# Optimization experiments

Hardware: AMD Instinct MI355X
Metric: run time of the kernel (lower is better)

## Reference

```python
import jax, jax.numpy as jnp
import numpy as np

N = 20000
IN_C = 512
HID = 64
H1 = 8
OUT_C = 256
E = 320000
NEG_SLOPE = 0.2


def gat_conv(x, src, dst, W, a_src, a_dst, b, concat):
    # PyG GATConv (shared lin for src/dst), inference mode (no dropout).
    H, C = a_src.shape
    h = (x @ W).reshape(N, H, C)                      # [N,H,C]
    alpha_src = (h * a_src[None]).sum(-1)             # [N,H]
    alpha_dst = (h * a_dst[None]).sum(-1)             # [N,H]
    alpha = jax.nn.leaky_relu(alpha_src[src] + alpha_dst[dst], NEG_SLOPE)  # [E,H]
    # segment softmax over incoming edges of each dst node
    amax = jax.ops.segment_max(alpha, dst, num_segments=N)
    amax = jnp.where(jnp.isfinite(amax), amax, 0.0)
    ex = jnp.exp(alpha - amax[dst])
    denom = jax.ops.segment_sum(ex, dst, num_segments=N)
    coef = ex / (denom[dst] + 1e-16)                  # [E,H]
    msg = h[src] * coef[:, :, None]                   # [E,H,C]
    out = jax.ops.segment_sum(msg, dst, num_segments=N)  # [N,H,C]
    out = out.reshape(N, H * C) if concat else out.mean(axis=1)
    return out + b


def setup_inputs() -> dict:
    key = jax.random.key(0)
    ks = jax.random.split(key, 10)
    x = jax.random.normal(ks[0], (N, IN_C), dtype=jnp.float32)
    edge_index = jax.random.randint(ks[1], (2, E), 0, N, dtype=jnp.int32)
    s1 = 1.0 / np.sqrt(IN_C)
    s2 = 1.0 / np.sqrt(HID * H1)
    W1 = jax.random.uniform(ks[2], (IN_C, H1 * HID), jnp.float32, -s1, s1)
    att_src1 = jax.random.uniform(ks[3], (H1, HID), jnp.float32, -s1, s1)
    att_dst1 = jax.random.uniform(ks[4], (H1, HID), jnp.float32, -s1, s1)
    b1 = jnp.zeros((H1 * HID,), jnp.float32)
    W2 = jax.random.uniform(ks[5], (H1 * HID, OUT_C), jnp.float32, -s2, s2)
    att_src2 = jax.random.uniform(ks[6], (1, OUT_C), jnp.float32, -s2, s2)
    att_dst2 = jax.random.uniform(ks[7], (1, OUT_C), jnp.float32, -s2, s2)
    b2 = jnp.zeros((OUT_C,), jnp.float32)
    return {"x": x, "edge_index": edge_index, "W1": W1, "att_src1": att_src1,
            "att_dst1": att_dst1, "b1": b1, "W2": W2, "att_src2": att_src2,
            "att_dst2": att_dst2, "b2": b2}


def reference(x, edge_index, W1, att_src1, att_dst1, b1, W2, att_src2, att_dst2, b2):
    # add self-loops (PyG GATConv default add_self_loops=True)
    loop = jnp.arange(N, dtype=edge_index.dtype)
    src = jnp.concatenate([edge_index[0], loop])
    dst = jnp.concatenate([edge_index[1], loop])
    h = gat_conv(x, src, dst, W1, att_src1, att_dst1, b1, concat=True)
    h = jax.nn.elu(h)
    out = gat_conv(h, src, dst, W2, att_src2, att_dst2, b2, concat=False)
    return jax.nn.log_softmax(out, axis=1)
```

## Files before the change

kernel.cpp:

```cpp
#include <hip/hip_runtime.h>
#include <math.h>

#define N_NODES 20000
#define NP1     20001
#define IN_CH   512
#define HID_TOT 512
#define OUT_CH  256
#define N_EDGE  320000
#define TOT_EDGE (N_EDGE + N_NODES)
#define EPAD    400000

typedef __attribute__((ext_vector_type(8))) short short8;
typedef __attribute__((ext_vector_type(4))) float f32x4;
typedef __attribute__((ext_vector_type(2))) float f32x2;

__device__ __forceinline__ ushort f2bf(float f) {
    union { float f; unsigned u; } v; v.f = f;
    unsigned u = v.u;
    return (ushort)((u + 0x7fffu + ((u >> 16) & 1u)) >> 16);
}

__device__ __forceinline__ void glds16(const ushort* g, ushort* l) {
    __builtin_amdgcn_global_load_lds(
        (const __attribute__((address_space(1))) void*)g,
        (__attribute__((address_space(3))) void*)l, 16, 0, 0);
}

__device__ __forceinline__ float lrelu(float a) { return fmaxf(a, 0.2f * a); }

#define NA_BLK (N_NODES * IN_CH / 4 / 256)
#define NB_BLK ((IN_CH / 64) * (HID_TOT / 4))
#define NC_BLK ((HID_TOT / 64) * (OUT_CH / 4))
#define NZ_BLK ((N_NODES + 255) / 256)
__global__ __launch_bounds__(256) void prep_kernel(const float* __restrict__ x,
                                                   ushort* __restrict__ xb,
                                                   const float* __restrict__ W1,
                                                   ushort* __restrict__ w1t,
                                                   const float* __restrict__ W2,
                                                   ushort* __restrict__ w2t,
                                                   int* __restrict__ counts,
                                                   float* __restrict__ as1,
                                                   float* __restrict__ as2,
                                                   float* __restrict__ ad2,
                                                   unsigned char* __restrict__ h1f,
                                                   unsigned char* __restrict__ h2f) {
    int b = blockIdx.x;
    int t = threadIdx.x;
    if (b < NA_BLK) {
        int i = b * 256 + t;
        float4 v = *(const float4*)&x[(size_t)i * 4];
        ushort4 o = make_ushort4(f2bf(v.x), f2bf(v.y), f2bf(v.z), f2bf(v.w));
        *(ushort4*)&xb[(size_t)i * 4] = o;
    } else if (b < NA_BLK + NB_BLK) {
        int bb = b - NA_BLK;
        int k = (bb & 7) * 64 + (t & 63);
        int n = (bb >> 3) * 4 + (t >> 6);
        w1t[(size_t)n * IN_CH + k] = f2bf(W1[(size_t)k * HID_TOT + n]);
    } else if (b < NA_BLK + NB_BLK + NC_BLK) {
        int bb = b - NA_BLK - NB_BLK;
        int k = (bb & 7) * 64 + (t & 63);
        int n = (bb >> 3) * 4 + (t >> 6);
        w2t[(size_t)n * HID_TOT + k] = f2bf(W2[(size_t)k * OUT_CH + n]);
    } else {
        int i = (b - NA_BLK - NB_BLK - NC_BLK) * 256 + t;
        if (i < N_NODES) { counts[i] = 0; as2[i] = 0.f; ad2[i] = 0.f; }
        if (i == N_NODES) as2[N_NODES] = -1e30f;
        if (i < 8) as1[(size_t)i * NP1 + N_NODES] = -1e30f;
        if (i < 128) ((unsigned*)(h1f + (size_t)N_NODES * HID_TOT))[i] = 0u;
        if (i < 64)  ((unsigned*)(h2f + (size_t)N_NODES * OUT_CH))[i] = 0u;
    }
}

__global__ void hist_kernel(const int* __restrict__ ei, int* __restrict__ counts) {
    int e = blockIdx.x * blockDim.x + threadIdx.x;
    if (e >= TOT_EDGE) return;
    int d = (e < N_EDGE) ? ei[N_EDGE + e] : (e - N_EDGE);
    atomicAdd(&counts[d], 1);
}

__global__ __launch_bounds__(1024) void scan_kernel(const int* __restrict__ counts,
                                                    int* __restrict__ offsets,
                                                    int* __restrict__ cursors,
                                                    int* __restrict__ srcs,
                                                    int* __restrict__ perm) {
    const int C = (N_NODES + 1023) / 1024;
    int t = threadIdx.x;
    int lane = t & 63, wid = t >> 6;
    int base = t * C;
    int sum = 0;
#pragma unroll
    for (int i = 0; i < C; i++) {
        int idx = base + i;
        if (idx < N_NODES) sum += (counts[idx] + 3) & ~3;
    }
    int val = sum;
#pragma unroll
    for (int off = 1; off < 64; off <<= 1) {
        int y = __shfl_up(val, off);
        if (lane >= off) val += y;
    }
    __shared__ int wsum[16], woff[16], stotal;
    __shared__ int bins[64];
    if (lane == 63) wsum[wid] = val;
    if (t < 64) bins[t] = 0;
    __syncthreads();
    if (t == 0) {
        int r = 0;
        for (int w = 0; w < 16; w++) { woff[w] = r; r += wsum[w]; }
        stotal = r;
    }
    __syncthreads();
    int running = woff[wid] + (val - sum);
#pragma unroll
    for (int i = 0; i < C; i++) {
        int idx = base + i;
        if (idx < N_NODES) {
            offsets[idx] = running;
            cursors[idx] = running;
            int real = counts[idx];
            int padded = (real + 3) & ~3;
            for (int pp = running + real; pp < running + padded; pp++)
                srcs[pp] = N_NODES;
            running += padded;
        }
    }
    if (t == 0) offsets[N_NODES] = stotal;

#pragma unroll
    for (int i = 0; i < C; i++) {
        int idx = base + i;
        if (idx < N_NODES) {
            int d = counts[idx]; if (d > 63) d = 63;
            atomicAdd(&bins[d], 1);
        }
    }
    __syncthreads();
    if (t == 0) {
        int r = 0;
        for (int d = 0; d < 64; d++) { int c = bins[d]; bins[d] = r; r += c; }
    }
    __syncthreads();
#pragma unroll
    for (int i = 0; i < C; i++) {
        int idx = base + i;
        if (idx < N_NODES) {
            int d = counts[idx]; if (d > 63) d = 63;
            int pos = atomicAdd(&bins[d], 1);
            perm[pos] = idx;
        }
    }
}

__global__ void scatter_kernel(const int* __restrict__ ei, int* __restrict__ cursors,
                               int* __restrict__ srcs) {
    int e = blockIdx.x * blockDim.x + threadIdx.x;
    if (e >= TOT_EDGE) return;
    int s, d;
    if (e < N_EDGE) { s = ei[e]; d = ei[N_EDGE + e]; } else { s = e - N_EDGE; d = s; }
    int pos = atomicAdd(&cursors[d], 1);
    srcs[pos] = s;
}

__global__ __launch_bounds__(256, 2) void gemm_mfma_kernel(const ushort* __restrict__ A,
                                                           const ushort* __restrict__ Bt,
                                                           unsigned char* __restrict__ Cf8,
                                                           const float* __restrict__ asrc,
                                                           const float* __restrict__ adst,
                                                           float* __restrict__ as_out,
                                                           float* __restrict__ ad_out,
                                                           int M, int N, int K, int layer1) {
    __shared__ ushort As[128 * 64];
    __shared__ ushort Bs[128 * 64];
    int t = threadIdx.x;
    int lane = t & 63;
    int wave = t >> 6;
    int wr = (wave >> 1) * 64;
    int wc = (wave & 1) * 64;
    int bm = blockIdx.y * 128, bn = blockIdx.x * 128;
    int q = lane >> 4, l15 = lane & 15;

    const ushort* Aptr[4]; ushort* Alds[4];
    const ushort* Bptr[4]; ushort* Blds[4];
#pragma unroll
    for (int k = 0; k < 4; k++) {
        int c = t + 256 * k;
        int r = c >> 3, kqs = c & 7;
        int kqg = kqs ^ (r & 7);
        int ar = bm + r; if (ar >= M) ar = M - 1;
        Aptr[k] = A + (size_t)ar * K + kqg * 8;
        Alds[k] = &As[c * 8];
        Bptr[k] = Bt + (size_t)(bn + r) * K + kqg * 8;
        Blds[k] = &Bs[c * 8];
    }

    f32x4 acc[4][4];
#pragma unroll
    for (int i = 0; i < 4; i++)
#pragma unroll
        for (int j = 0; j < 4; j++) acc[i][j] = f32x4{0.f, 0.f, 0.f, 0.f};

    for (int k0 = 0; k0 < K; k0 += 64) {
        __syncthreads();
        glds16(Aptr[0] + k0, Alds[0]);
        glds16(Aptr[1] + k0, Alds[1]);
        glds16(Aptr[2] + k0, Alds[2]);
        glds16(Aptr[3] + k0, Alds[3]);
        glds16(Bptr[0] + k0, Blds[0]);
        glds16(Bptr[1] + k0, Blds[1]);
        glds16(Bptr[2] + k0, Blds[2]);
        glds16(Bptr[3] + k0, Blds[3]);
        __syncthreads();

#pragma unroll
        for (int s = 0; s < 2; s++) {
            int kq = s * 4 + q;
            short8 af[4], bf[4];
#pragma unroll
            for (int i = 0; i < 4; i++) {
                int row = wr + i * 16 + l15;
                int slot = kq ^ (row & 7);
                af[i] = *(const short8*)&As[row * 64 + slot * 8];
            }
#pragma unroll
            for (int j = 0; j < 4; j++) {
                int row = wc + j * 16 + l15;
                int slot = kq ^ (row & 7);
                bf[j] = *(const short8*)&Bs[row * 64 + slot * 8];
            }
#pragma unroll
            for (int i = 0; i < 4; i++)
#pragma unroll
                for (int j = 0; j < 4; j++)
                    acc[i][j] = __builtin_amdgcn_mfma_f32_16x16x32_bf16(af[i], bf[j], acc[i][j], 0, 0, 0);
        }
    }

    float av[4], dv[4];
#pragma unroll
    for (int j = 0; j < 4; j++) {
        int cg = bn + wc + j * 16 + l15;
        av[j] = asrc[cg];
        dv[j] = adst[cg];
    }
    float ps[4][4], pd[4][4];
#pragma unroll
    for (int i = 0; i < 4; i++)
#pragma unroll
        for (int r = 0; r < 4; r++) {
            float p = 0.f, d = 0.f;
#pragma unroll
            for (int j = 0; j < 4; j++) {
                p = fmaf(acc[i][j][r], av[j], p);
                d = fmaf(acc[i][j][r], dv[j], d);
            }
            ps[i][r] = p; pd[i][r] = d;
        }
#pragma unroll
    for (int off = 1; off < 16; off <<= 1) {
#pragma unroll
        for (int i = 0; i < 4; i++)
#pragma unroll
            for (int r = 0; r < 4; r++) {
                ps[i][r] += __shfl_xor(ps[i][r], off);
                pd[i][r] += __shfl_xor(pd[i][r], off);
            }
    }

    int hidx = blockIdx.x * 2 + (wave & 1);
#pragma unroll
    for (int i = 0; i < 4; i++) {
#pragma unroll
        for (int r = 0; r < 4; r++) {
            int rg = bm + wr + i * 16 + q * 4 + r;
            if (rg < M) {
#pragma unroll
                for (int j = 0; j < 4; j++) {
                    int cg = bn + wc + j * 16 + l15;
                    int w8 = __builtin_amdgcn_cvt_pk_fp8_f32(acc[i][j][r], acc[i][j][r], 0, false);
                    Cf8[(size_t)rg * N + cg] = (unsigned char)(w8 & 0xff);
                }
                if (l15 == 0) {
                    if (layer1) {
                        as_out[(size_t)hidx * NP1 + rg] = ps[i][r];
                        ad_out[(size_t)hidx * NP1 + rg] = pd[i][r];
                    } else {
                        atomicAdd(&as_out[rg], ps[i][r]);
                        atomicAdd(&ad_out[rg], pd[i][r]);
                    }
                }
            }
        }
    }
}

__global__ __launch_bounds__(64) void agg1_kernel(const unsigned char* __restrict__ h1f,
                                                  const float* __restrict__ as1,
                                                  const float* __restrict__ ad1,
                                                  const int* __restrict__ offsets,
                                                  const int* __restrict__ srcs,
                                                  const int* __restrict__ perm,
                                                  const float* __restrict__ b1,
                                                  ushort* __restrict__ h1ab) {
    int b = blockIdx.x;
    int head = b & 7;
    int grp = b >> 3;
    int lane = threadIdx.x;
    int sub = lane >> 3;
    int l8 = lane & 7;
    int v = perm[grp * 8 + sub];
    int cofs = head * 64 + l8 * 8;
    const unsigned char* hb = h1f + cofs;
    const float* as1h = as1 + (size_t)head * NP1;
    float adv = ad1[(size_t)head * NP1 + v];
    int s = offsets[v], e = offsets[v + 1];

    float denom = 0.f;
    float acc[8];
#pragma unroll
    for (int k = 0; k < 8; k++) acc[k] = 0.f;

    int i = s;
    int4 cs0 = {0, 0, 0, 0}, cs1 = {0, 0, 0, 0};
    int csn = N_NODES;
    if (i + 8 <= e) {
        cs0 = *(const int4*)&srcs[i];
        cs1 = *(const int4*)&srcs[i + 4];
        csn = srcs[i + l8];
    }
    while (i + 8 <= e) {
        uint2 r[8];
        r[0] = *(const uint2*)&hb[(size_t)cs0.x * HID_TOT];
        r[1] = *(const uint2*)&hb[(size_t)cs0.y * HID_TOT];
        r[2] = *(const uint2*)&hb[(size_t)cs0.z * HID_TOT];
        r[3] = *(const uint2*)&hb[(size_t)cs0.w * HID_TOT];
        r[4] = *(const uint2*)&hb[(size_t)cs1.x * HID_TOT];
        r[5] = *(const uint2*)&hb[(size_t)cs1.y * HID_TOT];
        r[6] = *(const uint2*)&hb[(size_t)cs1.z * HID_TOT];
        r[7] = *(const uint2*)&hb[(size_t)cs1.w * HID_TOT];
        float aown = as1h[csn];
        int ni = i + 8;
        int4 ns0 = cs0, ns1 = cs1; int nsn = csn;
        if (ni + 8 <= e) {
            ns0 = *(const int4*)&srcs[ni];
            ns1 = *(const int4*)&srcs[ni + 4];
            nsn = srcs[ni + l8];
        }
        float w_own = __expf(lrelu(aown + adv));
        denom += w_own;
        float ww[8];
#pragma unroll
        for (int j = 0; j < 8; j++) ww[j] = __shfl(w_own, (lane & 56) | j);
#pragma unroll
        for (int j = 0; j < 8; j++) {
            f32x2 pa = __builtin_amdgcn_cvt_pk_f32_fp8(r[j].x, false);
            f32x2 pb = __builtin_amdgcn_cvt_pk_f32_fp8(r[j].x, true);
            f32x2 pc = __builtin_amdgcn_cvt_pk_f32_fp8(r[j].y, false);
            f32x2 pdd = __builtin_amdgcn_cvt_pk_f32_fp8(r[j].y, true);
            acc[0] = fmaf(ww[j], pa.x, acc[0]); acc[1] = fmaf(ww[j], pa.y, acc[1]);
            acc[2] = fmaf(ww[j], pb.x, acc[2]); acc[3] = fmaf(ww[j], pb.y, acc[3]);
            acc[4] = fmaf(ww[j], pc.x, acc[4]); acc[5] = fmaf(ww[j], pc.y, acc[5]);
            acc[6] = fmaf(ww[j], pdd.x, acc[6]); acc[7] = fmaf(ww[j], pdd.y, acc[7]);
        }
        cs0 = ns0; cs1 = ns1; csn = nsn; i = ni;
    }
    if (i < e) {
        int4 s0 = *(const int4*)&srcs[i];
        int snt = srcs[i + (l8 & 3)];
        uint2 r[4];
        r[0] = *(const uint2*)&hb[(size_t)s0.x * HID_TOT];
        r[1] = *(const uint2*)&hb[(size_t)s0.y * HID_TOT];
        r[2] = *(const uint2*)&hb[(size_t)s0.z * HID_TOT];
        r[3] = *(const uint2*)&hb[(size_t)s0.w * HID_TOT];
        float w_own = __expf(lrelu(as1h[snt] + adv));
        if (l8 < 4) denom += w_own;
        float ww[4];
#pragma unroll
        for (int j = 0; j < 4; j++) ww[j] = __shfl(w_own, (lane & 56) | j);
#pragma unroll
        for (int j = 0; j < 4; j++) {
            f32x2 pa = __builtin_amdgcn_cvt_pk_f32_fp8(r[j].x, false);
            f32x2 pb = __builtin_amdgcn_cvt_pk_f32_fp8(r[j].x, true);
            f32x2 pc = __builtin_amdgcn_cvt_pk_f32_fp8(r[j].y, false);
            f32x2 pdd = __builtin_amdgcn_cvt_pk_f32_fp8(r[j].y, true);
            acc[0] = fmaf(ww[j], pa.x, acc[0]); acc[1] = fmaf(ww[j], pa.y, acc[1]);
            acc[2] = fmaf(ww[j], pb.x, acc[2]); acc[3] = fmaf(ww[j], pb.y, acc[3]);
            acc[4] = fmaf(ww[j], pc.x, acc[4]); acc[5] = fmaf(ww[j], pc.y, acc[5]);
            acc[6] = fmaf(ww[j], pdd.x, acc[6]); acc[7] = fmaf(ww[j], pdd.y, acc[7]);
        }
    }

    denom += __shfl_xor(denom, 1);
    denom += __shfl_xor(denom, 2);
    denom += __shfl_xor(denom, 4);

    float inv = 1.f / (denom + 1e-16f);
    short8 ov;
#pragma unroll
    for (int k = 0; k < 8; k++) {
        float o = acc[k] * inv + b1[cofs + k];
        o = (o > 0.f) ? o : expm1f(o);
        ov[k] = (short)f2bf(o);
    }
    *(short8*)&h1ab[(size_t)v * HID_TOT + cofs] = ov;
}

__global__ __launch_bounds__(64) void agg2_kernel(const unsigned char* __restrict__ h2f,
                                                  const float* __restrict__ as2,
                                                  const float* __restrict__ ad2,
                                                  const int* __restrict__ offsets,
                                                  const int* __restrict__ srcs,
                                                  const int* __restrict__ perm,
                                                  const float* __restrict__ b2,
                                                  float* __restrict__ out) {
    int lane = threadIdx.x;
    int sub = lane >> 5;
    int l32 = lane & 31;
    int v = perm[blockIdx.x * 2 + sub];
    int c8 = l32 * 8;
    const unsigned char* hb = h2f + c8;
    float adv = ad2[v];
    int s = offsets[v], e = offsets[v + 1];

    float denom = 0.f;
    float acc[8];
#pragma unroll
    for (int k = 0; k < 8; k++) acc[k] = 0.f;

    int i = s;
    int4 cs0 = {0, 0, 0, 0}, cs1 = {0, 0, 0, 0};
    int csn = N_NODES;
    if (i + 8 <= e) {
        cs0 = *(const int4*)&srcs[i];
        cs1 = *(const int4*)&srcs[i + 4];
        csn = srcs[i + (l32 & 7)];
    }
    while (i + 8 <= e) {
        uint2 r[8];
        r[0] = *(const uint2*)&hb[(size_t)cs0.x * OUT_CH];
        r[1] = *(const uint2*)&hb[(size_t)cs0.y * OUT_CH];
        r[2] = *(const uint2*)&hb[(size_t)cs0.z * OUT_CH];
        r[3] = *(const uint2*)&hb[(size_t)cs0.w * OUT_CH];
        r[4] = *(const uint2*)&hb[(size_t)cs1.x * OUT_CH];
        r[5] = *(const uint2*)&hb[(size_t)cs1.y * OUT_CH];
        r[6] = *(const uint2*)&hb[(size_t)cs1.z * OUT_CH];
        r[7] = *(const uint2*)&hb[(size_t)cs1.w * OUT_CH];
        float aown = as2[csn];
        int ni = i + 8;
        int4 ns0 = cs0, ns1 = cs1; int nsn = csn;
        if (ni + 8 <= e) {
            ns0 = *(const int4*)&srcs[ni];
            ns1 = *(const int4*)&srcs[ni + 4];
            nsn = srcs[ni + (l32 & 7)];
        }
        float w_own = __expf(lrelu(aown + adv));
        if (l32 < 8) denom += w_own;
        float ww[8];
#pragma unroll
        for (int j = 0; j < 8; j++) ww[j] = __shfl(w_own, (lane & 32) | j);
#pragma unroll
        for (int j = 0; j < 8; j++) {
            f32x2 pa = __builtin_amdgcn_cvt_pk_f32_fp8(r[j].x, false);
            f32x2 pb = __builtin_amdgcn_cvt_pk_f32_fp8(r[j].x, true);
            f32x2 pc = __builtin_amdgcn_cvt_pk_f32_fp8(r[j].y, false);
            f32x2 pdd = __builtin_amdgcn_cvt_pk_f32_fp8(r[j].y, true);
            acc[0] = fmaf(ww[j], pa.x, acc[0]); acc[1] = fmaf(ww[j], pa.y, acc[1]);
            acc[2] = fmaf(ww[j], pb.x, acc[2]); acc[3] = fmaf(ww[j], pb.y, acc[3]);
            acc[4] = fmaf(ww[j], pc.x, acc[4]); acc[5] = fmaf(ww[j], pc.y, acc[5]);
            acc[6] = fmaf(ww[j], pdd.x, acc[6]); acc[7] = fmaf(ww[j], pdd.y, acc[7]);
        }
        cs0 = ns0; cs1 = ns1; csn = nsn; i = ni;
    }
    if (i < e) {
        int4 s0 = *(const int4*)&srcs[i];
        int snt = srcs[i + (l32 & 3)];
        uint2 r[4];
        r[0] = *(const uint2*)&hb[(size_t)s0.x * OUT_CH];
        r[1] = *(const uint2*)&hb[(size_t)s0.y * OUT_CH];
        r[2] = *(const uint2*)&hb[(size_t)s0.z * OUT_CH];
        r[3] = *(const uint2*)&hb[(size_t)s0.w * OUT_CH];
        float w_own = __expf(lrelu(as2[snt] + adv));
        if (l32 < 4) denom += w_own;
        float ww[4];
#pragma unroll
        for (int j = 0; j < 4; j++) ww[j] = __shfl(w_own, (lane & 32) | j);
#pragma unroll
        for (int j = 0; j < 4; j++) {
            f32x2 pa = __builtin_amdgcn_cvt_pk_f32_fp8(r[j].x, false);
            f32x2 pb = __builtin_amdgcn_cvt_pk_f32_fp8(r[j].x, true);
            f32x2 pc = __builtin_amdgcn_cvt_pk_f32_fp8(r[j].y, false);
            f32x2 pdd = __builtin_amdgcn_cvt_pk_f32_fp8(r[j].y, true);
            acc[0] = fmaf(ww[j], pa.x, acc[0]); acc[1] = fmaf(ww[j], pa.y, acc[1]);
            acc[2] = fmaf(ww[j], pb.x, acc[2]); acc[3] = fmaf(ww[j], pb.y, acc[3]);
            acc[4] = fmaf(ww[j], pc.x, acc[4]); acc[5] = fmaf(ww[j], pc.y, acc[5]);
            acc[6] = fmaf(ww[j], pdd.x, acc[6]); acc[7] = fmaf(ww[j], pdd.y, acc[7]);
        }
    }

    denom += __shfl_xor(denom, 1);
    denom += __shfl_xor(denom, 2);
    denom += __shfl_xor(denom, 4);
    denom += __shfl_xor(denom, 8);
    denom += __shfl_xor(denom, 16);

    float inv = 1.f / (denom + 1e-16f);
    float xv[8];
#pragma unroll
    for (int k = 0; k < 8; k++) xv[k] = acc[k] * inv + b2[c8 + k];

    float mm = xv[0];
#pragma unroll
    for (int k = 1; k < 8; k++) mm = fmaxf(mm, xv[k]);
#pragma unroll
    for (int off = 1; off < 32; off <<= 1) mm = fmaxf(mm, __shfl_xor(mm, off));
    float sum = 0.f;
#pragma unroll
    for (int k = 0; k < 8; k++) sum += __expf(xv[k] - mm);
#pragma unroll
    for (int off = 1; off < 32; off <<= 1) sum += __shfl_xor(sum, off);
    float ls = logf(sum);
    float4 o0, o1;
    o0.x = xv[0] - mm - ls; o0.y = xv[1] - mm - ls;
    o0.z = xv[2] - mm - ls; o0.w = xv[3] - mm - ls;
    o1.x = xv[4] - mm - ls; o1.y = xv[5] - mm - ls;
    o1.z = xv[6] - mm - ls; o1.w = xv[7] - mm - ls;
    *(float4*)&out[(size_t)v * OUT_CH + c8] = o0;
    *(float4*)&out[(size_t)v * OUT_CH + c8 + 4] = o1;
}

static inline size_t align256(size_t x) { return (x + 255) & ~(size_t)255; }

extern "C" void kernel_launch(void* const* d_in, const int* in_sizes, int n_in,
                              void* d_out, int out_size, void* d_ws, size_t ws_size,
                              hipStream_t stream) {
    const float* x    = (const float*)d_in[0];
    const int*   ei   = (const int*)d_in[1];
    const float* W1   = (const float*)d_in[2];
    const float* as1w = (const float*)d_in[3];
    const float* ad1w = (const float*)d_in[4];
    const float* b1   = (const float*)d_in[5];
    const float* W2   = (const float*)d_in[6];
    const float* as2w = (const float*)d_in[7];
    const float* ad2w = (const float*)d_in[8];
    const float* b2   = (const float*)d_in[9];
    float* out = (float*)d_out;

    char* p = (char*)d_ws;
    unsigned char* h1f = (unsigned char*)p; p += align256((size_t)NP1 * HID_TOT);
    unsigned char* h2f = (unsigned char*)p; p += align256((size_t)NP1 * OUT_CH);
    ushort* xb   = (ushort*)p; p += align256(sizeof(ushort) * (size_t)N_NODES * IN_CH);
    ushort* h1ab = xb;
    ushort* w1t  = (ushort*)p; p += align256(sizeof(ushort) * (size_t)IN_CH * HID_TOT);
    ushort* w2t  = (ushort*)p; p += align256(sizeof(ushort) * (size_t)HID_TOT * OUT_CH);
    float* as1  = (float*)p; p += align256(sizeof(float) * (size_t)NP1 * 8);
    float* ad1  = (float*)p; p += align256(sizeof(float) * (size_t)NP1 * 8);
    float* as2  = (float*)p; p += align256(sizeof(float) * (size_t)NP1);
    float* ad2  = (float*)p; p += align256(sizeof(float) * (size_t)NP1);
    int* counts  = (int*)p; p += align256(sizeof(int) * (size_t)N_NODES);
    int* offsets = (int*)p; p += align256(sizeof(int) * (size_t)(N_NODES + 1));
    int* cursors = (int*)p; p += align256(sizeof(int) * (size_t)N_NODES);
    int* perm    = (int*)p; p += align256(sizeof(int) * (size_t)N_NODES);
    int* srcs    = (int*)p; p += align256(sizeof(int) * (size_t)EPAD);

    prep_kernel<<<NA_BLK + NB_BLK + NC_BLK + NZ_BLK, 256, 0, stream>>>(
        x, xb, W1, w1t, W2, w2t, counts, as1, as2, ad2, h1f, h2f);

    int eb = (TOT_EDGE + 255) / 256;
    hist_kernel<<<eb, 256, 0, stream>>>(ei, counts);
    scan_kernel<<<1, 1024, 0, stream>>>(counts, offsets, cursors, srcs, perm);
    scatter_kernel<<<eb, 256, 0, stream>>>(ei, cursors, srcs);

    gemm_mfma_kernel<<<dim3(HID_TOT / 128, (N_NODES + 127) / 128), 256, 0, stream>>>(
        xb, w1t, h1f, as1w, ad1w, as1, ad1, N_NODES, HID_TOT, IN_CH, 1);
    agg1_kernel<<<2500 * 8, 64, 0, stream>>>(h1f, as1, ad1, offsets, srcs, perm, b1, h1ab);

    gemm_mfma_kernel<<<dim3(OUT_CH / 128, (N_NODES + 127) / 128), 256, 0, stream>>>(
        h1ab, w2t, h2f, as2w, ad2w, as2, ad2, N_NODES, OUT_CH, HID_TOT, 0);
    agg2_kernel<<<N_NODES / 2, 64, 0, stream>>>(h2f, as2, ad2, offsets, srcs, perm, b2, out);
}
```

Measured before the change: 305.2 us.

## Move degree binning and padding fill out of single-block scan into parallel kernels

The degree histogram, the degree-sorted permutation and the padding-slot fill used to run inside the single-block scan kernel. They now run in two new multi-block kernels: a block-local degree histogram reduced with global atomics, and a perm kernel that claims bin ranges atomically. This cuts serial work in the one-block scan but adds two kernel launches. Order within a bin is now nondeterministic, which only changes the processing order.

```diff
diff --git a/kernel.cpp b/kernel.cpp
--- a/kernel.cpp
+++ b/kernel.cpp
@@ -43,7 +43,8 @@
                                                    float* __restrict__ as2,
                                                    float* __restrict__ ad2,
                                                    unsigned char* __restrict__ h1f,
-                                                   unsigned char* __restrict__ h2f) {
+                                                   unsigned char* __restrict__ h2f,
+                                                   int* __restrict__ dbins) {
     int b = blockIdx.x;
     int t = threadIdx.x;
     if (b < NA_BLK) {
@@ -68,6 +69,7 @@
         if (i < 8) as1[(size_t)i * NP1 + N_NODES] = -1e30f;
         if (i < 128) ((unsigned*)(h1f + (size_t)N_NODES * HID_TOT))[i] = 0u;
         if (i < 64)  ((unsigned*)(h2f + (size_t)N_NODES * OUT_CH))[i] = 0u;
+        if (i >= 128 && i < 192) dbins[i - 128] = 0;
     }
 }
 
@@ -78,11 +80,26 @@
     atomicAdd(&counts[d], 1);
 }
 
+__global__ __launch_bounds__(256) void dhist_kernel(const int* __restrict__ counts,
+                                                    int* __restrict__ dbins) {
+    __shared__ int lb[64];
+    int t = threadIdx.x;
+    int v = blockIdx.x * 256 + t;
+    if (t < 64) lb[t] = 0;
+    __syncthreads();
+    if (v < N_NODES) {
+        int d = counts[v]; if (d > 63) d = 63;
+        atomicAdd(&lb[d], 1);
+    }
+    __syncthreads();
+    if (t < 64 && lb[t] > 0) atomicAdd(&dbins[t], lb[t]);
+}
+
 __global__ __launch_bounds__(1024) void scan_kernel(const int* __restrict__ counts,
                                                     int* __restrict__ offsets,
                                                     int* __restrict__ cursors,
-                                                    int* __restrict__ srcs,
-                                                    int* __restrict__ perm) {
+                                                    const int* __restrict__ dbins,
+                                                    int* __restrict__ binstart) {
     const int C = (N_NODES + 1023) / 1024;
     int t = threadIdx.x;
     int lane = t & 63, wid = t >> 6;
@@ -100,9 +117,7 @@
         if (lane >= off) val += y;
     }
     __shared__ int wsum[16], woff[16], stotal;
-    __shared__ int bins[64];
     if (lane == 63) wsum[wid] = val;
-    if (t < 64) bins[t] = 0;
     __syncthreads();
     if (t == 0) {
         int r = 0;
@@ -117,37 +132,40 @@
         if (idx < N_NODES) {
             offsets[idx] = running;
             cursors[idx] = running;
-            int real = counts[idx];
-            int padded = (real + 3) & ~3;
-            for (int pp = running + real; pp < running + padded; pp++)
-                srcs[pp] = N_NODES;
-            running += padded;
+            running += (counts[idx] + 3) & ~3;
         }
     }
     if (t == 0) offsets[N_NODES] = stotal;
-
-#pragma unroll
-    for (int i = 0; i < C; i++) {
-        int idx = base + i;
-        if (idx < N_NODES) {
-            int d = counts[idx]; if (d > 63) d = 63;
-            atomicAdd(&bins[d], 1);
-        }
-    }
+    if (t == 1) {
+        int r = 0;
+        for (int d = 0; d < 64; d++) { binstart[d] = r; r += dbins[d]; }
+    }
+}
+
+__global__ __launch_bounds__(256) void perm_kernel(const int* __restrict__ counts,
+                                                   const int* __restrict__ offsets,
+                                                   int* __restrict__ binstart,
+                                                   int* __restrict__ perm,
+                                                   int* __restrict__ srcs) {
+    __shared__ int lbins[64], lbase[64];
+    int t = threadIdx.x;
+    int v = blockIdx.x * 256 + t;
+    if (t < 64) lbins[t] = 0;
     __syncthreads();
-    if (t == 0) {
-        int r = 0;
-        for (int d = 0; d < 64; d++) { int c = bins[d]; bins[d] = r; r += c; }
+    int d = 0, lrank = 0;
+    bool valid = (v < N_NODES);
+    if (valid) {
+        d = counts[v]; if (d > 63) d = 63;
+        lrank = atomicAdd(&lbins[d], 1);
     }
     __syncthreads();
-#pragma unroll
-    for (int i = 0; i < C; i++) {
-        int idx = base + i;
-        if (idx < N_NODES) {
-            int d = counts[idx]; if (d > 63) d = 63;
-            int pos = atomicAdd(&bins[d], 1);
-            perm[pos] = idx;
-        }
+    if (t < 64 && lbins[t] > 0) lbase[t] = atomicAdd(&binstart[t], lbins[t]);
+    __syncthreads();
+    if (valid) {
+        perm[lbase[d] + lrank] = v;
+        int o = offsets[v], real = counts[v], padded = (real + 3) & ~3;
+        for (int pp = o + real; pp < o + padded; pp++)
+            srcs[pp] = N_NODES;
     }
 }
 
@@ -560,13 +578,17 @@
     int* cursors = (int*)p; p += align256(sizeof(int) * (size_t)N_NODES);
     int* perm    = (int*)p; p += align256(sizeof(int) * (size_t)N_NODES);
     int* srcs    = (int*)p; p += align256(sizeof(int) * (size_t)EPAD);
+    int* dbins   = (int*)p; p += align256(sizeof(int) * 64);
+    int* binstart= (int*)p; p += align256(sizeof(int) * 64);
 
     prep_kernel<<<NA_BLK + NB_BLK + NC_BLK + NZ_BLK, 256, 0, stream>>>(
-        x, xb, W1, w1t, W2, w2t, counts, as1, as2, ad2, h1f, h2f);
+        x, xb, W1, w1t, W2, w2t, counts, as1, as2, ad2, h1f, h2f, dbins);
 
     int eb = (TOT_EDGE + 255) / 256;
     hist_kernel<<<eb, 256, 0, stream>>>(ei, counts);
-    scan_kernel<<<1, 1024, 0, stream>>>(counts, offsets, cursors, srcs, perm);
+    dhist_kernel<<<NZ_BLK, 256, 0, stream>>>(counts, dbins);
+    scan_kernel<<<1, 1024, 0, stream>>>(counts, offsets, cursors, dbins, binstart);
+    perm_kernel<<<NZ_BLK, 256, 0, stream>>>(counts, offsets, binstart, perm, srcs);
     scatter_kernel<<<eb, 256, 0, stream>>>(ei, cursors, srcs);
 
     gemm_mfma_kernel<<<dim3(HID_TOT / 128, (N_NODES + 127) / 128), 256, 0, stream>>>(
```

Result: faster. 274.1 us (-10.2%).

## Relabel nodes by degree-sorted rank, head-major h1 layout, 16-bit source indices

Applied to the files above, without the earlier changes.

Nodes are renumbered by a per-256-segment degree sort, computed in a new parallel perm kernel, and all intermediate buffers are indexed by the new rank. That removes the perm indirection in the aggregation kernels and makes their accesses to offsets and attention scores sequential. Layer-1 features are stored head-major, so each head's gather touches a compact 64-byte-per-node table that can stay in cache, and the second GEMM reads that layout through a strided A pointer. Source indices shrink to ushort to halve index traffic, which relies on N fitting in 16 bits. The cost is extra invperm lookups in the scatter and the GEMM epilogue, plus a scattered final output write.

```diff
diff --git a/kernel.cpp b/kernel.cpp
--- a/kernel.cpp
+++ b/kernel.cpp
@@ -9,6 +9,7 @@
 #define N_EDGE  320000
 #define TOT_EDGE (N_EDGE + N_NODES)
 #define EPAD    400000
+#define NSEG    ((N_NODES + 255) / 256)
 
 typedef __attribute__((ext_vector_type(8))) short short8;
 typedef __attribute__((ext_vector_type(4))) float f32x4;
@@ -66,8 +67,10 @@
         if (i < N_NODES) { counts[i] = 0; as2[i] = 0.f; ad2[i] = 0.f; }
         if (i == N_NODES) as2[N_NODES] = -1e30f;
         if (i < 8) as1[(size_t)i * NP1 + N_NODES] = -1e30f;
-        if (i < 128) ((unsigned*)(h1f + (size_t)N_NODES * HID_TOT))[i] = 0u;
-        if (i < 64)  ((unsigned*)(h2f + (size_t)N_NODES * OUT_CH))[i] = 0u;
+        if (i < 128)
+            ((unsigned*)(h1f + ((size_t)(i >> 4) * NP1 + N_NODES) * 64))[i & 15] = 0u;
+        if (i < 64)
+            ((unsigned*)(h2f + (size_t)N_NODES * OUT_CH))[i] = 0u;
     }
 }
 
@@ -78,20 +81,50 @@
     atomicAdd(&counts[d], 1);
 }
 
+__global__ __launch_bounds__(256) void perm_kernel(const int* __restrict__ counts,
+                                                   int* __restrict__ perm,
+                                                   int* __restrict__ invperm) {
+    __shared__ int bins[64], starts[64];
+    int seg = blockIdx.x;
+    int t = threadIdx.x;
+    int v = seg * 256 + t;
+    bool valid = (v < N_NODES);
+    if (t < 64) bins[t] = 0;
+    __syncthreads();
+    int d = 0, rank = 0;
+    if (valid) {
+        d = counts[v]; if (d > 63) d = 63;
+        rank = atomicAdd(&bins[d], 1);
+    }
+    __syncthreads();
+    if (t == 0) {
+        int r = 0;
+        for (int k = 0; k < 64; k++) { starts[k] = r; r += bins[k]; }
+    }
+    __syncthreads();
+    if (valid) {
+        int pos = seg * 256 + starts[d] + rank;
+        perm[pos] = v;
+        invperm[v] = pos;
+    }
+}
+
 __global__ __launch_bounds__(1024) void scan_kernel(const int* __restrict__ counts,
+                                                    const int* __restrict__ perm,
                                                     int* __restrict__ offsets,
                                                     int* __restrict__ cursors,
-                                                    int* __restrict__ srcs,
-                                                    int* __restrict__ perm) {
+                                                    ushort* __restrict__ srcs) {
     const int C = (N_NODES + 1023) / 1024;
     int t = threadIdx.x;
     int lane = t & 63, wid = t >> 6;
     int base = t * C;
+    int cnt[C];
     int sum = 0;
 #pragma unroll
     for (int i = 0; i < C; i++) {
         int idx = base + i;
-        if (idx < N_NODES) sum += (counts[idx] + 3) & ~3;
+        cnt[i] = (idx < N_NODES) ? counts[perm[idx]] : 0;
+        sum += (cnt[i] + 3) & ~3;
     }
     int val = sum;
 #pragma unroll
@@ -100,9 +133,7 @@
         if (lane >= off) val += y;
     }
     __shared__ int wsum[16], woff[16], stotal;
-    __shared__ int bins[64];
     if (lane == 63) wsum[wid] = val;
-    if (t < 64) bins[t] = 0;
     __syncthreads();
     if (t == 0) {
         int r = 0;
@@ -117,48 +148,24 @@
         if (idx < N_NODES) {
             offsets[idx] = running;
             cursors[idx] = running;
-            int real = counts[idx];
-            int padded = (real + 3) & ~3;
+            int real = cnt[i], padded = (real + 3) & ~3;
             for (int pp = running + real; pp < running + padded; pp++)
-                srcs[pp] = N_NODES;
+                srcs[pp] = (ushort)N_NODES;
             running += padded;
         }
     }
     if (t == 0) offsets[N_NODES] = stotal;
-
-#pragma unroll
-    for (int i = 0; i < C; i++) {
-        int idx = base + i;
-        if (idx < N_NODES) {
-            int d = counts[idx]; if (d > 63) d = 63;
-            atomicAdd(&bins[d], 1);
-        }
-    }
-    __syncthreads();
-    if (t == 0) {
-        int r = 0;
-        for (int d = 0; d < 64; d++) { int c = bins[d]; bins[d] = r; r += c; }
-    }
-    __syncthreads();
-#pragma unroll
-    for (int i = 0; i < C; i++) {
-        int idx = base + i;
-        if (idx < N_NODES) {
-            int d = counts[idx]; if (d > 63) d = 63;
-            int pos = atomicAdd(&bins[d], 1);
-            perm[pos] = idx;
-        }
-    }
-}
-
-__global__ void scatter_kernel(const int* __restrict__ ei, int* __restrict__ cursors,
-                               int* __restrict__ srcs) {
+}
+
+__global__ void scatter_kernel(const int* __restrict__ ei, const int* __restrict__ invperm,
+                               int* __restrict__ cursors, ushort* __restrict__ srcs) {
     int e = blockIdx.x * blockDim.x + threadIdx.x;
     if (e >= TOT_EDGE) return;
     int s, d;
     if (e < N_EDGE) { s = ei[e]; d = ei[N_EDGE + e]; } else { s = e - N_EDGE; d = s; }
-    int pos = atomicAdd(&cursors[d], 1);
-    srcs[pos] = s;
+    int dr = invperm[d];
+    int pos = atomicAdd(&cursors[dr], 1);
+    srcs[pos] = (ushort)invperm[s];
 }
 
 __global__ __launch_bounds__(256, 2) void gemm_mfma_kernel(const ushort* __restrict__ A,
@@ -168,7 +175,9 @@
                                                            const float* __restrict__ adst,
                                                            float* __restrict__ as_out,
                                                            float* __restrict__ ad_out,
-                                                           int M, int N, int K, int layer1) {
+                                                           const int* __restrict__ invp,
+                                                           int M, int N, int K,
+                                                           int layer1, int aHM) {
     __shared__ ushort As[128 * 64];
     __shared__ ushort Bs[128 * 64];
     int t = threadIdx.x;
@@ -178,6 +187,7 @@
     int wc = (wave & 1) * 64;
     int bm = blockIdx.y * 128, bn = blockIdx.x * 128;
     int q = lane >> 4, l15 = lane & 15;
+    size_t kmul = aHM ? (size_t)NP1 : 1;
 
     const ushort* Aptr[4]; ushort* Alds[4];
     const ushort* Bptr[4]; ushort* Blds[4];
@@ -187,7 +197,8 @@
         int r = c >> 3, kqs = c & 7;
         int kqg = kqs ^ (r & 7);
         int ar = bm + r; if (ar >= M) ar = M - 1;
-        Aptr[k] = A + (size_t)ar * K + kqg * 8;
+        Aptr[k] = aHM ? (A + (size_t)ar * 64 + kqg * 8)
+                      : (A + (size_t)ar * K + kqg * 8);
         Alds[k] = &As[c * 8];
         Bptr[k] = Bt + (size_t)(bn + r) * K + kqg * 8;
         Blds[k] = &Bs[c * 8];
@@ -201,10 +212,10 @@
 
     for (int k0 = 0; k0 < K; k0 += 64) {
         __syncthreads();
-        glds16(Aptr[0] + k0, Alds[0]);
-        glds16(Aptr[1] + k0, Alds[1]);
-        glds16(Aptr[2] + k0, Alds[2]);
-        glds16(Aptr[3] + k0, Alds[3]);
+        glds16(Aptr[0] + (size_t)k0 * kmul, Alds[0]);
+        glds16(Aptr[1] + (size_t)k0 * kmul, Alds[1]);
+        glds16(Aptr[2] + (size_t)k0 * kmul, Alds[2]);
+        glds16(Aptr[3] + (size_t)k0 * kmul, Alds[3]);
         glds16(Bptr[0] + k0, Blds[0]);
         glds16(Bptr[1] + k0, Blds[1]);
         glds16(Bptr[2] + k0, Blds[2]);
@@ -273,17 +284,25 @@
         for (int r = 0; r < 4; r++) {
             int rg = bm + wr + i * 16 + q * 4 + r;
             if (rg < M) {
-#pragma unroll
-                for (int j = 0; j < 4; j++) {
-                    int cg = bn + wc + j * 16 + l15;
-                    int w8 = __builtin_amdgcn_cvt_pk_fp8_f32(acc[i][j][r], acc[i][j][r], 0, false);
-                    Cf8[(size_t)rg * N + cg] = (unsigned char)(w8 & 0xff);
-                }
-                if (l15 == 0) {
-                    if (layer1) {
-                        as_out[(size_t)hidx * NP1 + rg] = ps[i][r];
-                        ad_out[(size_t)hidx * NP1 + rg] = pd[i][r];
-                    } else {
+                if (layer1) {
+                    int rr = invp[rg];
+#pragma unroll
+                    for (int j = 0; j < 4; j++) {
+                        int w8 = __builtin_amdgcn_cvt_pk_fp8_f32(acc[i][j][r], acc[i][j][r], 0, false);
+                        Cf8[((size_t)hidx * NP1 + rr) * 64 + j * 16 + l15] = (unsigned char)(w8 & 0xff);
+                    }
+                    if (l15 == 0) {
+                        as_out[(size_t)hidx * NP1 + rr] = ps[i][r];
+                        ad_out[(size_t)hidx * NP1 + rr] = pd[i][r];
+                    }
+                } else {
+#pragma unroll
+                    for (int j = 0; j < 4; j++) {
+                        int cg = bn + wc + j * 16 + l15;
+                        int w8 = __builtin_amdgcn_cvt_pk_fp8_f32(acc[i][j][r], acc[i][j][r], 0, false);
+                        Cf8[(size_t)rg * N + cg] = (unsigned char)(w8 & 0xff);
+                    }
+                    if (l15 == 0) {
                         atomicAdd(&as_out[rg], ps[i][r]);
                         atomicAdd(&ad_out[rg], pd[i][r]);
                     }
@@ -297,8 +316,7 @@
                                                   const float* __restrict__ as1,
                                                   const float* __restrict__ ad1,
                                                   const int* __restrict__ offsets,
-                                                  const int* __restrict__ srcs,
-                                                  const int* __restrict__ perm,
+                                                  const ushort* __restrict__ srcs,
                                                   const float* __restrict__ b1,
                                                   ushort* __restrict__ h1ab) {
     int b = blockIdx.x;
@@ -307,12 +325,12 @@
     int lane = threadIdx.x;
     int sub = lane >> 3;
     int l8 = lane & 7;
-    int v = perm[grp * 8 + sub];
+    int rk = grp * 8 + sub;
     int cofs = head * 64 + l8 * 8;
-    const unsigned char* hb = h1f + cofs;
+    const unsigned char* hb = h1f + (size_t)head * NP1 * 64 + l8 * 8;
     const float* as1h = as1 + (size_t)head * NP1;
-    float adv = ad1[(size_t)head * NP1 + v];
-    int s = offsets[v], e = offsets[v + 1];
+    float adv = ad1[(size_t)head * NP1 + rk];
+    int s = offsets[rk], e = offsets[rk + 1];
 
     float denom = 0.f;
     float acc[8];
@@ -320,29 +338,28 @@
     for (int k = 0; k < 8; k++) acc[k] = 0.f;
 
     int i = s;
-    int4 cs0 = {0, 0, 0, 0}, cs1 = {0, 0, 0, 0};
+    uint2 ca = {0u, 0u}, cb = {0u, 0u};
     int csn = N_NODES;
     if (i + 8 <= e) {
-        cs0 = *(const int4*)&srcs[i];
-        cs1 = *(const int4*)&srcs[i + 4];
+        ca = *(const uint2*)&srcs[i];
+        cb = *(const uint2*)&srcs[i + 4];
         csn = srcs[i + l8];
     }
     while (i + 8 <= e) {
+        int sn[8] = {(int)(ca.x & 0xffff), (int)(ca.x >> 16),
+                     (int)(ca.y & 0xffff), (int)(ca.y >> 16),
+                     (int)(cb.x & 0xffff), (int)(cb.x >> 16),
+                     (int)(cb.y & 0xffff), (int)(cb.y >> 16)};
         uint2 r[8];
-        r[0] = *(const uint2*)&hb[(size_t)cs0.x * HID_TOT];
-        r[1] = *(const uint2*)&hb[(size_t)cs0.y * HID_TOT];
-        r[2] = *(const uint2*)&hb[(size_t)cs0.z * HID_TOT];
-        r[3] = *(const uint2*)&hb[(size_t)cs0.w * HID_TOT];
-        r[4] = *(const uint2*)&hb[(size_t)cs1.x * HID_TOT];
-        r[5] = *(const uint2*)&hb[(size_t)cs1.y * HID_TOT];
-        r[6] = *(const uint2*)&hb[(size_t)cs1.z * HID_TOT];
-        r[7] = *(const uint2*)&hb[(size_t)cs1.w * HID_TOT];
+#pragma unroll
+        for (int j = 0; j < 8; j++)
+            r[j] = *(const uint2*)&hb[(size_t)sn[j] * 64];
         float aown = as1h[csn];
         int ni = i + 8;
-        int4 ns0 = cs0, ns1 = cs1; int nsn = csn;
+        uint2 na = ca, nb = cb; int nsn = csn;
         if (ni + 8 <= e) {
-            ns0 = *(const int4*)&srcs[ni];
-            ns1 = *(const int4*)&srcs[ni + 4];
+            na = *(const uint2*)&srcs[ni];
+            nb = *(const uint2*)&srcs[ni + 4];
             nsn = srcs[ni + l8];
         }
         float w_own = __expf(lrelu(aown + adv));
@@ -361,16 +378,17 @@
             acc[4] = fmaf(ww[j], pc.x, acc[4]); acc[5] = fmaf(ww[j], pc.y, acc[5]);
             acc[6] = fmaf(ww[j], pdd.x, acc[6]); acc[7] = fmaf(ww[j], pdd.y, acc[7]);
         }
-        cs0 = ns0; cs1 = ns1; csn = nsn; i = ni;
+        ca = na; cb = nb; csn = nsn; i = ni;
     }
     if (i < e) {
-        int4 s0 = *(const int4*)&srcs[i];
+        uint2 pa4 = *(const uint2*)&srcs[i];
+        int sn[4] = {(int)(pa4.x & 0xffff), (int)(pa4.x >> 16),
+                     (int)(pa4.y & 0xffff), (int)(pa4.y >> 16)};
         int snt = srcs[i + (l8 & 3)];
         uint2 r[4];
-        r[0] = *(const uint2*)&hb[(size_t)s0.x * HID_TOT];
-        r[1] = *(const uint2*)&hb[(size_t)s0.y * HID_TOT];
-        r[2] = *(const uint2*)&hb[(size_t)s0.z * HID_TOT];
-        r[3] = *(const uint2*)&hb[(size_t)s0.w * HID_TOT];
+#pragma unroll
+        for (int j = 0; j < 4; j++)
+            r[j] = *(const uint2*)&hb[(size_t)sn[j] * 64];
         float w_own = __expf(lrelu(as1h[snt] + adv));
         if (l8 < 4) denom += w_own;
         float ww[4];
@@ -401,25 +419,25 @@
         o = (o > 0.f) ? o : expm1f(o);
         ov[k] = (short)f2bf(o);
     }
-    *(short8*)&h1ab[(size_t)v * HID_TOT + cofs] = ov;
+    *(short8*)&h1ab[((size_t)head * NP1 + rk) * 64 + l8 * 8] = ov;
 }
 
 __global__ __launch_bounds__(64) void agg2_kernel(const unsigned char* __restrict__ h2f,
                                                   const float* __restrict__ as2,
                                                   const float* __restrict__ ad2,
                                                   const int* __restrict__ offsets,
-                                                  const int* __restrict__ srcs,
+                                                  const ushort* __restrict__ srcs,
                                                   const int* __restrict__ perm,
                                                   const float* __restrict__ b2,
                                                   float* __restrict__ out) {
     int lane = threadIdx.x;
     int sub = lane >> 5;
     int l32 = lane & 31;
-    int v = perm[blockIdx.x * 2 + sub];
+    int rk = blockIdx.x * 2 + sub;
     int c8 = l32 * 8;
     const unsigned char* hb = h2f + c8;
-    float adv = ad2[v];
-    int s = offsets[v], e = offsets[v + 1];
+    float adv = ad2[rk];
+    int s = offsets[rk], e = offsets[rk + 1];
 
     float denom = 0.f;
     float acc[8];
@@ -427,29 +445,28 @@
     for (int k = 0; k < 8; k++) acc[k] = 0.f;
 
     int i = s;
-    int4 cs0 = {0, 0, 0, 0}, cs1 = {0, 0, 0, 0};
+    uint2 ca = {0u, 0u}, cb = {0u, 0u};
     int csn = N_NODES;
     if (i + 8 <= e) {
-        cs0 = *(const int4*)&srcs[i];
-        cs1 = *(const int4*)&srcs[i + 4];
+        ca = *(const uint2*)&srcs[i];
+        cb = *(const uint2*)&srcs[i + 4];
         csn = srcs[i + (l32 & 7)];
     }
     while (i + 8 <= e) {
+        int sn[8] = {(int)(ca.x & 0xffff), (int)(ca.x >> 16),
+                     (int)(ca.y & 0xffff), (int)(ca.y >> 16),
+                     (int)(cb.x & 0xffff), (int)(cb.x >> 16),
+                     (int)(cb.y & 0xffff), (int)(cb.y >> 16)};
         uint2 r[8];
-        r[0] = *(const uint2*)&hb[(size_t)cs0.x * OUT_CH];
-        r[1] = *(const uint2*)&hb[(size_t)cs0.y * OUT_CH];
-        r[2] = *(const uint2*)&hb[(size_t)cs0.z * OUT_CH];
-        r[3] = *(const uint2*)&hb[(size_t)cs0.w * OUT_CH];
-        r[4] = *(const uint2*)&hb[(size_t)cs1.x * OUT_CH];
-        r[5] = *(const uint2*)&hb[(size_t)cs1.y * OUT_CH];
-        r[6] = *(const uint2*)&hb[(size_t)cs1.z * OUT_CH];
-        r[7] = *(const uint2*)&hb[(size_t)cs1.w * OUT_CH];
+#pragma unroll
+        for (int j = 0; j < 8; j++)
+            r[j] = *(const uint2*)&hb[(size_t)sn[j] * OUT_CH];
         float aown = as2[csn];
         int ni = i + 8;
-        int4 ns0 = cs0, ns1 = cs1; int nsn = csn;
+        uint2 na = ca, nb = cb; int nsn = csn;
         if (ni + 8 <= e) {
-            ns0 = *(const int4*)&srcs[ni];
-            ns1 = *(const int4*)&srcs[ni + 4];
+            na = *(const uint2*)&srcs[ni];
+            nb = *(const uint2*)&srcs[ni + 4];
             nsn = srcs[ni + (l32 & 7)];
         }
         float w_own = __expf(lrelu(aown + adv));
@@ -468,16 +485,17 @@
             acc[4] = fmaf(ww[j], pc.x, acc[4]); acc[5] = fmaf(ww[j], pc.y, acc[5]);
             acc[6] = fmaf(ww[j], pdd.x, acc[6]); acc[7] = fmaf(ww[j], pdd.y, acc[7]);
         }
-        cs0 = ns0; cs1 = ns1; csn = nsn; i = ni;
+        ca = na; cb = nb; csn = nsn; i = ni;
     }
     if (i < e) {
-        int4 s0 = *(const int4*)&srcs[i];
+        uint2 pa4 = *(const uint2*)&srcs[i];
+        int sn[4] = {(int)(pa4.x & 0xffff), (int)(pa4.x >> 16),
+                     (int)(pa4.y & 0xffff), (int)(pa4.y >> 16)};
         int snt = srcs[i + (l32 & 3)];
         uint2 r[4];
-        r[0] = *(const uint2*)&hb[(size_t)s0.x * OUT_CH];
-        r[1] = *(const uint2*)&hb[(size_t)s0.y * OUT_CH];
-        r[2] = *(const uint2*)&hb[(size_t)s0.z * OUT_CH];
-        r[3] = *(const uint2*)&hb[(size_t)s0.w * OUT_CH];
+#pragma unroll
+        for (int j = 0; j < 4; j++)
+            r[j] = *(const uint2*)&hb[(size_t)sn[j] * OUT_CH];
         float w_own = __expf(lrelu(as2[snt] + adv));
         if (l32 < 4) denom += w_own;
         float ww[4];
@@ -518,13 +536,14 @@
 #pragma unroll
     for (int off = 1; off < 32; off <<= 1) sum += __shfl_xor(sum, off);
     float ls = logf(sum);
+    int vorig = perm[rk];
     float4 o0, o1;
     o0.x = xv[0] - mm - ls; o0.y = xv[1] - mm - ls;
     o0.z = xv[2] - mm - ls; o0.w = xv[3] - mm - ls;
     o1.x = xv[4] - mm - ls; o1.y = xv[5] - mm - ls;
     o1.z = xv[6] - mm - ls; o1.w = xv[7] - mm - ls;
-    *(float4*)&out[(size_t)v * OUT_CH + c8] = o0;
-    *(float4*)&out[(size_t)v * OUT_CH + c8 + 4] = o1;
+    *(float4*)&out[(size_t)vorig * OUT_CH + c8] = o0;
+    *(float4*)&out[(size_t)vorig * OUT_CH + c8 + 4] = o1;
 }
 
 static inline size_t align256(size_t x) { return (x + 255) & ~(size_t)255; }
@@ -545,9 +564,9 @@
     float* out = (float*)d_out;
 
     char* p = (char*)d_ws;
-    unsigned char* h1f = (unsigned char*)p; p += align256((size_t)NP1 * HID_TOT);
+    unsigned char* h1f = (unsigned char*)p; p += align256((size_t)8 * NP1 * 64);
     unsigned char* h2f = (unsigned char*)p; p += align256((size_t)NP1 * OUT_CH);
-    ushort* xb   = (ushort*)p; p += align256(sizeof(ushort) * (size_t)N_NODES * IN_CH);
+    ushort* xb   = (ushort*)p; p += align256(sizeof(ushort) * (size_t)8 * NP1 * 64);
     ushort* h1ab = xb;
     ushort* w1t  = (ushort*)p; p += align256(sizeof(ushort) * (size_t)IN_CH * HID_TOT);
     ushort* w2t  = (ushort*)p; p += align256(sizeof(ushort) * (size_t)HID_TOT * OUT_CH);
@@ -559,21 +578,23 @@
     int* offsets = (int*)p; p += align256(sizeof(int) * (size_t)(N_NODES + 1));
     int* cursors = (int*)p; p += align256(sizeof(int) * (size_t)N_NODES);
     int* perm    = (int*)p; p += align256(sizeof(int) * (size_t)N_NODES);
-    int* srcs    = (int*)p; p += align256(sizeof(int) * (size_t)EPAD);
+    int* invperm = (int*)p; p += align256(sizeof(int) * (size_t)N_NODES);
+    ushort* srcs = (ushort*)p; p += align256(sizeof(ushort) * (size_t)EPAD);
 
     prep_kernel<<<NA_BLK + NB_BLK + NC_BLK + NZ_BLK, 256, 0, stream>>>(
         x, xb, W1, w1t, W2, w2t, counts, as1, as2, ad2, h1f, h2f);
 
     int eb = (TOT_EDGE + 255) / 256;
     hist_kernel<<<eb, 256, 0, stream>>>(ei, counts);
-    scan_kernel<<<1, 1024, 0, stream>>>(counts, offsets, cursors, srcs, perm);
-    scatter_kernel<<<eb, 256, 0, stream>>>(ei, cursors, srcs);
+    perm_kernel<<<NSEG, 256, 0, stream>>>(counts, perm, invperm);
+    scan_kernel<<<1, 1024, 0, stream>>>(counts, perm, offsets, cursors, srcs);
+    scatter_kernel<<<eb, 256, 0, stream>>>(ei, invperm, cursors, srcs);
 
     gemm_mfma_kernel<<<dim3(HID_TOT / 128, (N_NODES + 127) / 128), 256, 0, stream>>>(
-        xb, w1t, h1f, as1w, ad1w, as1, ad1, N_NODES, HID_TOT, IN_CH, 1);
-    agg1_kernel<<<2500 * 8, 64, 0, stream>>>(h1f, as1, ad1, offsets, srcs, perm, b1, h1ab);
+        xb, w1t, h1f, as1w, ad1w, as1, ad1, invperm, N_NODES, HID_TOT, IN_CH, 1, 0);
+    agg1_kernel<<<2500 * 8, 64, 0, stream>>>(h1f, as1, ad1, offsets, srcs, b1, h1ab);
 
     gemm_mfma_kernel<<<dim3(OUT_CH / 128, (N_NODES + 127) / 128), 256, 0, stream>>>(
-        h1ab, w2t, h2f, as2w, ad2w, as2, ad2, N_NODES, OUT_CH, HID_TOT, 0);
+        h1ab, w2t, h2f, as2w, ad2w, as2, ad2, invperm, N_NODES, OUT_CH, HID_TOT, 0, 1);
     agg2_kernel<<<N_NODES / 2, 64, 0, stream>>>(h2f, as2, ad2, offsets, srcs, perm, b2, out);
 }
```

New measurement: 282.8 us. 1.08x faster.
